# Kernel optimization log

Hardware: AMD Instinct MI355X
Metric: run time of the kernel (lower is better)

Reference implementation:

```python
import jax, jax.numpy as jnp
import numpy as np

N_U = 100000   # user nodes
N_V = 100000   # item nodes
D = 64         # input_dim
O = 64         # output_dim
R = 5          # num_support (rating levels)
E = 500000     # edges per relation


def setup_inputs() -> dict:
    key = jax.random.key(0)
    ks = jax.random.split(key, 8)
    init_range = np.sqrt(6.0 / (D + O))
    return {
        "x_u": jax.random.normal(ks[0], (N_U, D), jnp.float32),
        "x_v": jax.random.normal(ks[1], (N_V, D), jnp.float32),
        "weights_u": jax.random.uniform(ks[2], (R, D, O), jnp.float32, -init_range, init_range),
        "weights_v": jax.random.uniform(ks[3], (R, D, O), jnp.float32, -init_range, init_range),
        "bias_u": jnp.full((O,), 0.01, jnp.float32),
        "bias_v": jnp.full((O,), 0.01, jnp.float32),
        "edge_val": jax.random.uniform(ks[4], (R, E), jnp.float32),
        "edge_u": jax.random.randint(ks[5], (R, E), 0, N_U, jnp.int32),
        "edge_v": jax.random.randint(ks[6], (R, E), 0, N_V, jnp.int32),
    }


def reference(x_u, x_v, weights_u, weights_v, bias_u, bias_v, edge_val, edge_u, edge_v):
    # Cumulative (ordinal mixture) weights: wu_i = sum_{j<=i} W_u[j]
    Wu = jnp.cumsum(weights_u, axis=0)          # [R, D, O]
    Wv = jnp.cumsum(weights_v, axis=0)          # [R, D, O]

    tmp_u = jnp.einsum("nd,rdo->rno", x_u, Wu)  # [R, N_U, O]
    tmp_v = jnp.einsum("md,rdo->rmo", x_v, Wv)  # [R, N_V, O]

    gather = jax.vmap(lambda t, idx: t[idx])    # per-relation row gather

    # z_u = sum_r support_r @ tmp_v_r : scatter edge messages into user rows
    msg_u = (edge_val[..., None] * gather(tmp_v, edge_v)).reshape(R * E, O)
    z_u = jax.ops.segment_sum(msg_u, edge_u.reshape(-1), num_segments=N_U)

    # z_v = sum_r support_r^T @ tmp_u_r : scatter into item rows
    msg_v = (edge_val[..., None] * gather(tmp_u, edge_u)).reshape(R * E, O)
    z_v = jax.ops.segment_sum(msg_v, edge_v.reshape(-1), num_segments=N_V)

    u_out = jax.nn.relu(z_u + bias_u)
    v_out = jax.nn.relu(z_v + bias_v)
    return (u_out, v_out)
```

## Files before the change

kernel.cpp:

```cpp
#include <hip/hip_runtime.h>

#define N_U 100000
#define N_V 100000
#define OO 64
#define RR 5
#define EE 500000
#define TOT_E (RR * EE)
#define NB 782
#define CAP 4096
#define CAPU 3584

typedef short bf16x8 __attribute__((ext_vector_type(8)));
typedef float f32x4 __attribute__((ext_vector_type(4)));

__device__ __forceinline__ float bf2f(unsigned short u) {
  union { unsigned int i; float f; } x;
  x.i = ((unsigned int)u) << 16;
  return x.f;
}
__device__ __forceinline__ unsigned short f2bf(float f) {
  union { float f; unsigned int i; } x;
  x.f = f;
  unsigned int lsb = (x.i >> 16) & 1u;
  unsigned int r = x.i + 0x7fffu + lsb;
  return (unsigned short)(r >> 16);
}

__global__ void prep_weights(const float* __restrict__ wu,
                             const float* __restrict__ wv,
                             unsigned short* __restrict__ bfrag) {
  int side = blockIdx.x;
  const float* w = side ? wv : wu;
  for (int idx = threadIdx.x; idx < 4096; idx += 256) {
    int d = idx >> 6, o = idx & 63;
    int c = o >> 4, n = o & 15;
    int sk = d >> 5, q = (d >> 3) & 3, jj = d & 7;
    int f = c * 2 + sk;
    int lane = q * 16 + n;
    int pos = (f * 64 + lane) * 8 + jj;
    float acc = 0.f;
    for (int r = 0; r < RR; ++r) {
      acc += w[r * 4096 + idx];
      bfrag[(side * RR + r) * 4096 + pos] = f2bf(acc);
    }
  }
}

__global__ __launch_bounds__(256) void gemm5_kernel(
    const float* __restrict__ X,
    const unsigned short* __restrict__ bfrag_side,
    unsigned short* __restrict__ tmp5) {
  __shared__ unsigned short smem[RR * 4096];
  for (int idx = threadIdx.x; idx < RR * 4096; idx += 256)
    smem[idx] = bfrag_side[idx];
  __syncthreads();

  int lane = threadIdx.x & 63;
  int wave = threadIdx.x >> 6;
  int q = lane >> 4, m = lane & 15;
  int t = blockIdx.x * 4 + wave;
  if (t >= N_U / 16) return;
  int r0 = t * 16;

  const float* xr = X + (size_t)(r0 + m) * 64;
  float4 p0 = *(const float4*)(xr + q * 8);
  float4 p1 = *(const float4*)(xr + q * 8 + 4);
  float4 p2 = *(const float4*)(xr + 32 + q * 8);
  float4 p3 = *(const float4*)(xr + 32 + q * 8 + 4);
  bf16x8 a0, a1;
  a0[0] = (short)f2bf(p0.x); a0[1] = (short)f2bf(p0.y);
  a0[2] = (short)f2bf(p0.z); a0[3] = (short)f2bf(p0.w);
  a0[4] = (short)f2bf(p1.x); a0[5] = (short)f2bf(p1.y);
  a0[6] = (short)f2bf(p1.z); a0[7] = (short)f2bf(p1.w);
  a1[0] = (short)f2bf(p2.x); a1[1] = (short)f2bf(p2.y);
  a1[2] = (short)f2bf(p2.z); a1[3] = (short)f2bf(p2.w);
  a1[4] = (short)f2bf(p3.x); a1[5] = (short)f2bf(p3.y);
  a1[6] = (short)f2bf(p3.z); a1[7] = (short)f2bf(p3.w);

  for (int r = 0; r < RR; ++r) {
    f32x4 acc[4];
#pragma unroll
    for (int c = 0; c < 4; ++c) {
      bf16x8 b0 = *(const bf16x8*)(smem + r * 4096 + ((c * 2 + 0) * 64 + lane) * 8);
      bf16x8 b1 = *(const bf16x8*)(smem + r * 4096 + ((c * 2 + 1) * 64 + lane) * 8);
      f32x4 a = {0.f, 0.f, 0.f, 0.f};
      a = __builtin_amdgcn_mfma_f32_16x16x32_bf16(a0, b0, a, 0, 0, 0);
      a = __builtin_amdgcn_mfma_f32_16x16x32_bf16(a1, b1, a, 0, 0, 0);
      acc[c] = a;
    }
    unsigned short* trow = tmp5 + (size_t)r * N_U * 64;
#pragma unroll
    for (int i = 0; i < 4; ++i) {
      ushort4 o;
      o.x = f2bf(acc[0][i]); o.y = f2bf(acc[1][i]);
      o.z = f2bf(acc[2][i]); o.w = f2bf(acc[3][i]);
      *(ushort4*)(trow + (size_t)(r0 + q * 4 + i) * 64 + m * 4) = o;
    }
  }
}

__global__ void init_cursor(unsigned* __restrict__ g) {
  int i = blockIdx.x * 256 + threadIdx.x;
  if (i < NB) g[i] = (unsigned)i * CAP;
}

__global__ __launch_bounds__(1024) void bucket_scatter(
    const int* __restrict__ dst, const int* __restrict__ src,
    const float* __restrict__ val, unsigned* __restrict__ gcursor,
    unsigned* __restrict__ keyP, unsigned short* __restrict__ valP) {
  __shared__ unsigned skey[8192];
  __shared__ unsigned short sval[8192];
  __shared__ unsigned short sbid[8192];
  __shared__ unsigned cnt[NB];
  __shared__ unsigned sc[1024];
  __shared__ unsigned gbase[NB];
  int tid = threadIdx.x;
  for (int i = tid; i < NB; i += 1024) cnt[i] = 0u;
  __syncthreads();
  int base = blockIdx.x * 8192;
  int t8 = base + tid * 8;
  bool full = (t8 < TOT_E);
  if (full) {
    int4 d0 = *(const int4*)(dst + t8);
    int4 d1 = *(const int4*)(dst + t8 + 4);
    atomicAdd(&cnt[d0.x >> 7], 1u);
    atomicAdd(&cnt[d0.y >> 7], 1u);
    atomicAdd(&cnt[d0.z >> 7], 1u);
    atomicAdd(&cnt[d0.w >> 7], 1u);
    atomicAdd(&cnt[d1.x >> 7], 1u);
    atomicAdd(&cnt[d1.y >> 7], 1u);
    atomicAdd(&cnt[d1.z >> 7], 1u);
    atomicAdd(&cnt[d1.w >> 7], 1u);
  }
  __syncthreads();
  sc[tid] = (tid < NB) ? cnt[tid] : 0u;
  __syncthreads();
  for (int off = 1; off < 1024; off <<= 1) {
    unsigned a = sc[tid];
    unsigned b = (tid >= off) ? sc[tid - off] : 0u;
    __syncthreads();
    sc[tid] = a + b;
    __syncthreads();
  }
  for (int b = tid; b < NB; b += 1024) {
    unsigned c = cnt[b];
    gbase[b] = c ? atomicAdd(&gcursor[b], c) : 0u;
    cnt[b] = sc[b] - c;
  }
  __syncthreads();
  unsigned total = sc[NB - 1];
  __syncthreads();
  for (int b = tid; b < NB; b += 1024) sc[b] = cnt[b];
  __syncthreads();
  if (full) {
    int4 d0 = *(const int4*)(dst + t8);
    int4 d1 = *(const int4*)(dst + t8 + 4);
    int4 s0 = *(const int4*)(src + t8);
    int4 s1 = *(const int4*)(src + t8 + 4);
    float4 v0 = *(const float4*)(val + t8);
    float4 v1 = *(const float4*)(val + t8 + 4);
    unsigned rb = (unsigned)(t8 / EE) * N_U;
#define PUT(dd, ss, vv)                                                     \
    {                                                                       \
      int bb = (dd) >> 7;                                                   \
      unsigned pos = atomicAdd(&sc[bb], 1u);                                \
      skey[pos] = (((unsigned)((dd) & 127)) << 19) | (rb + (unsigned)(ss)); \
      sval[pos] = f2bf(vv);                                                 \
      sbid[pos] = (unsigned short)bb;                                       \
    }
    PUT(d0.x, s0.x, v0.x)
    PUT(d0.y, s0.y, v0.y)
    PUT(d0.z, s0.z, v0.z)
    PUT(d0.w, s0.w, v0.w)
    PUT(d1.x, s1.x, v1.x)
    PUT(d1.y, s1.y, v1.y)
    PUT(d1.z, s1.z, v1.z)
    PUT(d1.w, s1.w, v1.w)
#undef PUT
  }
  __syncthreads();
  for (int i = tid; i < (int)total; i += 1024) {
    unsigned b = sbid[i];
    unsigned addr = gbase[b] + ((unsigned)i - cnt[b]);
    keyP[addr] = skey[i];
    valP[addr] = sval[i];
  }
}

__global__ __launch_bounds__(512, 8) void bucket_sort_agg(
    const unsigned* __restrict__ keyP, const unsigned short* __restrict__ valP,
    const unsigned* __restrict__ gcursor,
    const unsigned short* __restrict__ tmp5,
    const float* __restrict__ bias, float* __restrict__ out) {
  __shared__ unsigned okey[CAP];
  __shared__ unsigned short oval[CAP];
  __shared__ unsigned hist[128];
  __shared__ unsigned starts[129];
  __shared__ unsigned cur[128];
  int b = blockIdx.x;
  unsigned base = (unsigned)b * CAP;
  int cnt = (int)(gcursor[b] - base);
  if (cnt > CAPU) cnt = CAPU;
  for (int i = threadIdx.x; i < 128; i += 512) hist[i] = 0u;
  __syncthreads();
  for (int i = threadIdx.x; i < cnt; i += 512)
    atomicAdd(&hist[keyP[base + i] >> 19], 1u);
  __syncthreads();
  if (threadIdx.x == 0) {
    unsigned acc = 0u;
    for (int l = 0; l < 128; ++l) {
      starts[l] = acc;
      acc += (hist[l] + 3u) & ~3u;
    }
    starts[128] = acc;
  }
  __syncthreads();
  unsigned tot = starts[128];
  for (int i = threadIdx.x; i < (int)tot; i += 512) { okey[i] = 0u; oval[i] = 0; }
  for (int l = threadIdx.x; l < 128; l += 512) cur[l] = starts[l];
  __syncthreads();
  for (int i = threadIdx.x; i < cnt; i += 512) {
    unsigned k = keyP[base + i];
    unsigned pos = atomicAdd(&cur[k >> 19], 1u);
    okey[pos] = k & 0x7FFFFu;
    oval[pos] = valP[base + i];
  }
  __syncthreads();

  int lane = threadIdx.x & 63;
  int wave = threadIdx.x >> 6;
  int g16 = lane >> 4;
  int m = lane & 15;
  int nb0 = b * 128;
  int nodes = (N_U - nb0 < 128) ? (N_U - nb0) : 128;
  const unsigned short* tp = tmp5 + (m << 2);
  float bl = bias[lane];
  for (int l = wave; l < nodes; l += 8) {
    unsigned s = starts[l];
    unsigned e = starts[l + 1];
    float a0 = 0.f, a1 = 0.f, a2 = 0.f, a3 = 0.f;
    unsigned k = s;
    for (; k + 8 <= e; k += 8) {
      unsigned key0 = okey[k + g16];
      unsigned key1 = okey[k + 4 + g16];
      float v0 = bf2f(oval[k + g16]);
      float v1 = bf2f(oval[k + 4 + g16]);
      ushort4 t0 = *(const ushort4*)(tp + (size_t)key0 * 64);
      ushort4 t1 = *(const ushort4*)(tp + (size_t)key1 * 64);
      a0 += v0 * bf2f(t0.x);
      a1 += v0 * bf2f(t0.y);
      a2 += v0 * bf2f(t0.z);
      a3 += v0 * bf2f(t0.w);
      a0 += v1 * bf2f(t1.x);
      a1 += v1 * bf2f(t1.y);
      a2 += v1 * bf2f(t1.z);
      a3 += v1 * bf2f(t1.w);
    }
    if (k < e) {
      unsigned key0 = okey[k + g16];
      float v0 = bf2f(oval[k + g16]);
      ushort4 t0 = *(const ushort4*)(tp + (size_t)key0 * 64);
      a0 += v0 * bf2f(t0.x);
      a1 += v0 * bf2f(t0.y);
      a2 += v0 * bf2f(t0.z);
      a3 += v0 * bf2f(t0.w);
    }
    a0 += __shfl_xor(a0, 16); a0 += __shfl_xor(a0, 32);
    a1 += __shfl_xor(a1, 16); a1 += __shfl_xor(a1, 32);
    a2 += __shfl_xor(a2, 16); a2 += __shfl_xor(a2, 32);
    a3 += __shfl_xor(a3, 16); a3 += __shfl_xor(a3, 32);
    float r = (g16 & 2) ? ((g16 & 1) ? a3 : a2) : ((g16 & 1) ? a1 : a0);
    out[(size_t)(nb0 + l) * 64 + lane] = fmaxf(r + bl, 0.f);
  }
}

__global__ __launch_bounds__(256) void gemm_kernel(
    const float* __restrict__ X, const unsigned short* __restrict__ bfrag,
    unsigned short* __restrict__ tmp) {
  int lane = threadIdx.x & 63;
  int wave = threadIdx.x >> 6;
  int q = lane >> 4, m = lane & 15;
  bf16x8 bf[8];
#pragma unroll
  for (int f = 0; f < 8; ++f)
    bf[f] = *(const bf16x8*)(bfrag + (f * 64 + lane) * 8);
  int t = blockIdx.x * 4 + wave;
  if (t >= N_U / 16) return;
  int r0 = t * 16;
  const float* xr = X + (size_t)(r0 + m) * 64;
  float4 p0 = *(const float4*)(xr + q * 8);
  float4 p1 = *(const float4*)(xr + q * 8 + 4);
  float4 p2 = *(const float4*)(xr + 32 + q * 8);
  float4 p3 = *(const float4*)(xr + 32 + q * 8 + 4);
  bf16x8 a0, a1;
  a0[0] = (short)f2bf(p0.x); a0[1] = (short)f2bf(p0.y);
  a0[2] = (short)f2bf(p0.z); a0[3] = (short)f2bf(p0.w);
  a0[4] = (short)f2bf(p1.x); a0[5] = (short)f2bf(p1.y);
  a0[6] = (short)f2bf(p1.z); a0[7] = (short)f2bf(p1.w);
  a1[0] = (short)f2bf(p2.x); a1[1] = (short)f2bf(p2.y);
  a1[2] = (short)f2bf(p2.z); a1[3] = (short)f2bf(p2.w);
  a1[4] = (short)f2bf(p3.x); a1[5] = (short)f2bf(p3.y);
  a1[6] = (short)f2bf(p3.z); a1[7] = (short)f2bf(p3.w);
#pragma unroll
  for (int c = 0; c < 4; ++c) {
    f32x4 acc = {0.f, 0.f, 0.f, 0.f};
    acc = __builtin_amdgcn_mfma_f32_16x16x32_bf16(a0, bf[c * 2 + 0], acc, 0, 0, 0);
    acc = __builtin_amdgcn_mfma_f32_16x16x32_bf16(a1, bf[c * 2 + 1], acc, 0, 0, 0);
#pragma unroll
    for (int i = 0; i < 4; ++i)
      tmp[(size_t)(r0 + q * 4 + i) * 64 + c * 16 + m] = f2bf(acc[i]);
  }
}

__global__ __launch_bounds__(256) void scatter_kernel(
    const unsigned short* __restrict__ tmp, const float* __restrict__ edge_val,
    const int* __restrict__ dst_idx, const int* __restrict__ src_idx,
    float* __restrict__ z, int base, int cnt) {
  int e = blockIdx.x * 4 + (threadIdx.x >> 6);
  int j = threadIdx.x & 63;
  int d = dst_idx[e] - base;
  if ((unsigned)d >= (unsigned)cnt) return;
  int s = src_idx[e];
  float w = edge_val[e];
  atomicAdd(&z[(size_t)d * 64 + j], w * bf2f(tmp[(size_t)s * 64 + j]));
}

__global__ __launch_bounds__(256) void finalize_kernel(
    const float* __restrict__ z, const float* __restrict__ bias,
    float* __restrict__ out) {
  size_t i4 = ((size_t)blockIdx.x * 256 + threadIdx.x) * 4;
  float4 zz = *(const float4*)(z + i4);
  const float4 bb = *(const float4*)(bias + (i4 & 63));
  float4 o;
  o.x = fmaxf(zz.x + bb.x, 0.f);
  o.y = fmaxf(zz.y + bb.y, 0.f);
  o.z = fmaxf(zz.z + bb.z, 0.f);
  o.w = fmaxf(zz.w + bb.w, 0.f);
  *(float4*)(out + i4) = o;
}

extern "C" void kernel_launch(void* const* d_in, const int* in_sizes, int n_in,
                              void* d_out, int out_size, void* d_ws, size_t ws_size,
                              hipStream_t stream) {
  const float* x_u      = (const float*)d_in[0];
  const float* x_v      = (const float*)d_in[1];
  const float* w_u      = (const float*)d_in[2];
  const float* w_v      = (const float*)d_in[3];
  const float* bias_u   = (const float*)d_in[4];
  const float* bias_v   = (const float*)d_in[5];
  const float* edge_val = (const float*)d_in[6];
  const int*   edge_u   = (const int*)d_in[7];
  const int*   edge_v   = (const int*)d_in[8];
  float* out = (float*)d_out;
  char* ws = (char*)d_ws;

  const size_t FAST_NEED = 83763200;

  unsigned short* bfrag = (unsigned short*)ws;
  prep_weights<<<2, 256, 0, stream>>>(w_u, w_v, bfrag);

  if (ws_size >= FAST_NEED) {
    unsigned short* tmp5      = (unsigned short*)(ws + 131072);
    unsigned*       gcursor   = (unsigned*)(ws + 64131072);
    unsigned*       keyP      = (unsigned*)(ws + 64544768);
    unsigned short* valP      = (unsigned short*)(ws + 77357056);

    const int edge_grid = (TOT_E + 8191) / 8192;
    const int gemm_grid = (N_U / 16 + 3) / 4;

    for (int side = 0; side < 2; ++side) {
      const float* X = side ? x_u : x_v;
      const unsigned short* frag0 = bfrag + (side ? 0 : RR * 4096);
      const int* dst = side ? edge_v : edge_u;
      const int* src = side ? edge_u : edge_v;
      const float* bias = side ? bias_v : bias_u;
      float* out_side = out + (size_t)side * N_U * OO;

      init_cursor<<<4, 256, 0, stream>>>(gcursor);
      bucket_scatter<<<edge_grid, 1024, 0, stream>>>(dst, src, edge_val, gcursor,
                                                     keyP, valP);
      gemm5_kernel<<<gemm_grid, 256, 0, stream>>>(X, frag0, tmp5);
      bucket_sort_agg<<<NB, 512, 0, stream>>>(keyP, valP, gcursor, tmp5, bias,
                                              out_side);
    }
    return;
  }

  unsigned short* tmp = (unsigned short*)(ws + 131072);
  float*          z   = (float*)(ws + 131072 + 12800000);
  const size_t fixed = 131072 + 12800000;
  size_t zbytes = ws_size > fixed ? ws_size - fixed : 0;
  long chunk = (long)(zbytes / (OO * 4));
  chunk -= chunk % 16;
  if (chunk < 16) chunk = 16;
  if (chunk > N_U) chunk = N_U;

  const int gemm_grid = (N_U / 16 + 3) / 4;
  const int scat_grid = EE / 4;

  for (int side = 0; side < 2; ++side) {
    const float* X = side ? x_u : x_v;
    const unsigned short* frag0 = bfrag + (side ? 0 : RR * 4096);
    const int* dst = side ? edge_v : edge_u;
    const int* src = side ? edge_u : edge_v;
    const float* bias = side ? bias_v : bias_u;
    float* out_side = out + (size_t)side * N_U * OO;

    for (long base = 0; base < N_U; base += chunk) {
      long cnt = N_U - base < chunk ? N_U - base : chunk;
      hipMemsetAsync(z, 0, (size_t)cnt * OO * 4, stream);
      for (int r = 0; r < RR; ++r) {
        gemm_kernel<<<gemm_grid, 256, 0, stream>>>(X, frag0 + r * 4096, tmp);
        scatter_kernel<<<scat_grid, 256, 0, stream>>>(
            tmp, edge_val + (size_t)r * EE, dst + (size_t)r * EE,
            src + (size_t)r * EE, z, (int)base, (int)cnt);
      }
      finalize_kernel<<<(int)(cnt / 16), 256, 0, stream>>>(
          z, bias, out_side + base * OO);
    }
  }
}
```

Baseline: 337.9 us.

## Fuse bucket scatter and GEMM into one heterogeneous launch, fold cursor init

Merges the edge bucket-scatter kernel and the per-relation GEMM into a single launch: the first 306 blocks do the scatter and the rest run the MFMA GEMM with 1024-thread blocks of 16 waves. Cursor initialisation for both sides moves into prep_weights, using a separate cursor array per side, so the per-side init launches go away. This removes launch gaps and lets the memory-bound scatter overlap with the GEMM. The cost is that GEMM blocks now hold the larger shared-memory allocation and 1024 threads, which may reduce occupancy.

```diff
diff --git a/kernel.cpp b/kernel.cpp
--- a/kernel.cpp
+++ b/kernel.cpp
@@ -9,6 +9,8 @@
 #define NB 782
 #define CAP 4096
 #define CAPU 3584
+#define SCAT_BLOCKS 306
+#define GEMM_BLOCKS 391
 
 typedef short bf16x8 __attribute__((ext_vector_type(8)));
 typedef float f32x4 __attribute__((ext_vector_type(4)));
@@ -28,8 +30,13 @@
 
 __global__ void prep_weights(const float* __restrict__ wu,
                              const float* __restrict__ wv,
-                             unsigned short* __restrict__ bfrag) {
+                             unsigned short* __restrict__ bfrag,
+                             unsigned* __restrict__ gcur) {
   int side = blockIdx.x;
+  if (gcur) {
+    unsigned* g = gcur + side * 1024;
+    for (int i = threadIdx.x; i < NB; i += 256) g[i] = (unsigned)i * CAP;
+  }
   const float* w = side ? wv : wu;
   for (int idx = threadIdx.x; idx < 4096; idx += 256) {
     int d = idx >> 6, o = idx & 63;
@@ -46,144 +53,138 @@
   }
 }
 
-__global__ __launch_bounds__(256) void gemm5_kernel(
+__global__ __launch_bounds__(1024) void scatter_gemm(
+    const int* __restrict__ dst, const int* __restrict__ src,
+    const float* __restrict__ val, unsigned* __restrict__ gcursor,
+    unsigned* __restrict__ keyP, unsigned short* __restrict__ valP,
     const float* __restrict__ X,
     const unsigned short* __restrict__ bfrag_side,
     unsigned short* __restrict__ tmp5) {
-  __shared__ unsigned short smem[RR * 4096];
-  for (int idx = threadIdx.x; idx < RR * 4096; idx += 256)
-    smem[idx] = bfrag_side[idx];
-  __syncthreads();
-
-  int lane = threadIdx.x & 63;
-  int wave = threadIdx.x >> 6;
-  int q = lane >> 4, m = lane & 15;
-  int t = blockIdx.x * 4 + wave;
-  if (t >= N_U / 16) return;
-  int r0 = t * 16;
-
-  const float* xr = X + (size_t)(r0 + m) * 64;
-  float4 p0 = *(const float4*)(xr + q * 8);
-  float4 p1 = *(const float4*)(xr + q * 8 + 4);
-  float4 p2 = *(const float4*)(xr + 32 + q * 8);
-  float4 p3 = *(const float4*)(xr + 32 + q * 8 + 4);
-  bf16x8 a0, a1;
-  a0[0] = (short)f2bf(p0.x); a0[1] = (short)f2bf(p0.y);
-  a0[2] = (short)f2bf(p0.z); a0[3] = (short)f2bf(p0.w);
-  a0[4] = (short)f2bf(p1.x); a0[5] = (short)f2bf(p1.y);
-  a0[6] = (short)f2bf(p1.z); a0[7] = (short)f2bf(p1.w);
-  a1[0] = (short)f2bf(p2.x); a1[1] = (short)f2bf(p2.y);
-  a1[2] = (short)f2bf(p2.z); a1[3] = (short)f2bf(p2.w);
-  a1[4] = (short)f2bf(p3.x); a1[5] = (short)f2bf(p3.y);
-  a1[6] = (short)f2bf(p3.z); a1[7] = (short)f2bf(p3.w);
-
-  for (int r = 0; r < RR; ++r) {
-    f32x4 acc[4];
+  __shared__ unsigned lds_u32[18972];
+  int blk = blockIdx.x;
+  int tid = threadIdx.x;
+  if (blk < SCAT_BLOCKS) {
+    unsigned* skey = lds_u32;
+    unsigned short* sval = (unsigned short*)(lds_u32 + 8192);
+    unsigned short* sbid = (unsigned short*)(lds_u32 + 12288);
+    unsigned* cnt  = lds_u32 + 16384;
+    unsigned* sc   = lds_u32 + 17166;
+    unsigned* gbase = lds_u32 + 18190;
+    for (int i = tid; i < NB; i += 1024) cnt[i] = 0u;
+    __syncthreads();
+    int base = blk * 8192;
+    int t8 = base + tid * 8;
+    bool full = (t8 < TOT_E);
+    if (full) {
+      int4 d0 = *(const int4*)(dst + t8);
+      int4 d1 = *(const int4*)(dst + t8 + 4);
+      atomicAdd(&cnt[d0.x >> 7], 1u);
+      atomicAdd(&cnt[d0.y >> 7], 1u);
+      atomicAdd(&cnt[d0.z >> 7], 1u);
+      atomicAdd(&cnt[d0.w >> 7], 1u);
+      atomicAdd(&cnt[d1.x >> 7], 1u);
+      atomicAdd(&cnt[d1.y >> 7], 1u);
+      atomicAdd(&cnt[d1.z >> 7], 1u);
+      atomicAdd(&cnt[d1.w >> 7], 1u);
+    }
+    __syncthreads();
+    sc[tid] = (tid < NB) ? cnt[tid] : 0u;
+    __syncthreads();
+    for (int off = 1; off < 1024; off <<= 1) {
+      unsigned a = sc[tid];
+      unsigned b = (tid >= off) ? sc[tid - off] : 0u;
+      __syncthreads();
+      sc[tid] = a + b;
+      __syncthreads();
+    }
+    for (int b = tid; b < NB; b += 1024) {
+      unsigned c = cnt[b];
+      gbase[b] = c ? atomicAdd(&gcursor[b], c) : 0u;
+      cnt[b] = sc[b] - c;
+    }
+    __syncthreads();
+    unsigned total = sc[NB - 1];
+    __syncthreads();
+    for (int b = tid; b < NB; b += 1024) sc[b] = cnt[b];
+    __syncthreads();
+    if (full) {
+      int4 d0 = *(const int4*)(dst + t8);
+      int4 d1 = *(const int4*)(dst + t8 + 4);
+      int4 s0 = *(const int4*)(src + t8);
+      int4 s1 = *(const int4*)(src + t8 + 4);
+      float4 v0 = *(const float4*)(val + t8);
+      float4 v1 = *(const float4*)(val + t8 + 4);
+      unsigned rb = (unsigned)(t8 / EE) * N_U;
+#define PUT(dd, ss, vv)                                                     \
+      {                                                                     \
+        int bb = (dd) >> 7;                                                 \
+        unsigned pos = atomicAdd(&sc[bb], 1u);                              \
+        skey[pos] = (((unsigned)((dd) & 127)) << 19) | (rb + (unsigned)(ss)); \
+        sval[pos] = f2bf(vv);                                               \
+        sbid[pos] = (unsigned short)bb;                                     \
+      }
+      PUT(d0.x, s0.x, v0.x)
+      PUT(d0.y, s0.y, v0.y)
+      PUT(d0.z, s0.z, v0.z)
+      PUT(d0.w, s0.w, v0.w)
+      PUT(d1.x, s1.x, v1.x)
+      PUT(d1.y, s1.y, v1.y)
+      PUT(d1.z, s1.z, v1.z)
+      PUT(d1.w, s1.w, v1.w)
+#undef PUT
+    }
+    __syncthreads();
+    for (int i = tid; i < (int)total; i += 1024) {
+      unsigned b = sbid[i];
+      unsigned addr = gbase[b] + ((unsigned)i - cnt[b]);
+      keyP[addr] = skey[i];
+      valP[addr] = sval[i];
+    }
+  } else {
+    unsigned short* smem = (unsigned short*)lds_u32;
+    for (int i = tid; i < 2560; i += 1024)
+      ((bf16x8*)smem)[i] = ((const bf16x8*)bfrag_side)[i];
+    __syncthreads();
+    int lane = tid & 63;
+    int wave = tid >> 6;
+    int q = lane >> 4, m = lane & 15;
+    int t = (blk - SCAT_BLOCKS) * 16 + wave;
+    if (t >= N_U / 16) return;
+    int r0 = t * 16;
+    const float* xr = X + (size_t)(r0 + m) * 64;
+    float4 p0 = *(const float4*)(xr + q * 8);
+    float4 p1 = *(const float4*)(xr + q * 8 + 4);
+    float4 p2 = *(const float4*)(xr + 32 + q * 8);
+    float4 p3 = *(const float4*)(xr + 32 + q * 8 + 4);
+    bf16x8 a0, a1;
+    a0[0] = (short)f2bf(p0.x); a0[1] = (short)f2bf(p0.y);
+    a0[2] = (short)f2bf(p0.z); a0[3] = (short)f2bf(p0.w);
+    a0[4] = (short)f2bf(p1.x); a0[5] = (short)f2bf(p1.y);
+    a0[6] = (short)f2bf(p1.z); a0[7] = (short)f2bf(p1.w);
+    a1[0] = (short)f2bf(p2.x); a1[1] = (short)f2bf(p2.y);
+    a1[2] = (short)f2bf(p2.z); a1[3] = (short)f2bf(p2.w);
+    a1[4] = (short)f2bf(p3.x); a1[5] = (short)f2bf(p3.y);
+    a1[6] = (short)f2bf(p3.z); a1[7] = (short)f2bf(p3.w);
+    for (int r = 0; r < RR; ++r) {
+      f32x4 acc[4];
 #pragma unroll
-    for (int c = 0; c < 4; ++c) {
-      bf16x8 b0 = *(const bf16x8*)(smem + r * 4096 + ((c * 2 + 0) * 64 + lane) * 8);
-      bf16x8 b1 = *(const bf16x8*)(smem + r * 4096 + ((c * 2 + 1) * 64 + lane) * 8);
-      f32x4 a = {0.f, 0.f, 0.f, 0.f};
-      a = __builtin_amdgcn_mfma_f32_16x16x32_bf16(a0, b0, a, 0, 0, 0);
-      a = __builtin_amdgcn_mfma_f32_16x16x32_bf16(a1, b1, a, 0, 0, 0);
-      acc[c] = a;
-    }
-    unsigned short* trow = tmp5 + (size_t)r * N_U * 64;
+      for (int c = 0; c < 4; ++c) {
+        bf16x8 b0 = *(const bf16x8*)(smem + r * 4096 + ((c * 2 + 0) * 64 + lane) * 8);
+        bf16x8 b1 = *(const bf16x8*)(smem + r * 4096 + ((c * 2 + 1) * 64 + lane) * 8);
+        f32x4 a = {0.f, 0.f, 0.f, 0.f};
+        a = __builtin_amdgcn_mfma_f32_16x16x32_bf16(a0, b0, a, 0, 0, 0);
+        a = __builtin_amdgcn_mfma_f32_16x16x32_bf16(a1, b1, a, 0, 0, 0);
+        acc[c] = a;
+      }
+      unsigned short* trow = tmp5 + (size_t)r * N_U * 64;
 #pragma unroll
-    for (int i = 0; i < 4; ++i) {
-      ushort4 o;
-      o.x = f2bf(acc[0][i]); o.y = f2bf(acc[1][i]);
-      o.z = f2bf(acc[2][i]); o.w = f2bf(acc[3][i]);
-      *(ushort4*)(trow + (size_t)(r0 + q * 4 + i) * 64 + m * 4) = o;
-    }
-  }
-}
-
-__global__ void init_cursor(unsigned* __restrict__ g) {
-  int i = blockIdx.x * 256 + threadIdx.x;
-  if (i < NB) g[i] = (unsigned)i * CAP;
-}
-
-__global__ __launch_bounds__(1024) void bucket_scatter(
-    const int* __restrict__ dst, const int* __restrict__ src,
-    const float* __restrict__ val, unsigned* __restrict__ gcursor,
-    unsigned* __restrict__ keyP, unsigned short* __restrict__ valP) {
-  __shared__ unsigned skey[8192];
-  __shared__ unsigned short sval[8192];
-  __shared__ unsigned short sbid[8192];
-  __shared__ unsigned cnt[NB];
-  __shared__ unsigned sc[1024];
-  __shared__ unsigned gbase[NB];
-  int tid = threadIdx.x;
-  for (int i = tid; i < NB; i += 1024) cnt[i] = 0u;
-  __syncthreads();
-  int base = blockIdx.x * 8192;
-  int t8 = base + tid * 8;
-  bool full = (t8 < TOT_E);
-  if (full) {
-    int4 d0 = *(const int4*)(dst + t8);
-    int4 d1 = *(const int4*)(dst + t8 + 4);
-    atomicAdd(&cnt[d0.x >> 7], 1u);
-    atomicAdd(&cnt[d0.y >> 7], 1u);
-    atomicAdd(&cnt[d0.z >> 7], 1u);
-    atomicAdd(&cnt[d0.w >> 7], 1u);
-    atomicAdd(&cnt[d1.x >> 7], 1u);
-    atomicAdd(&cnt[d1.y >> 7], 1u);
-    atomicAdd(&cnt[d1.z >> 7], 1u);
-    atomicAdd(&cnt[d1.w >> 7], 1u);
-  }
-  __syncthreads();
-  sc[tid] = (tid < NB) ? cnt[tid] : 0u;
-  __syncthreads();
-  for (int off = 1; off < 1024; off <<= 1) {
-    unsigned a = sc[tid];
-    unsigned b = (tid >= off) ? sc[tid - off] : 0u;
-    __syncthreads();
-    sc[tid] = a + b;
-    __syncthreads();
-  }
-  for (int b = tid; b < NB; b += 1024) {
-    unsigned c = cnt[b];
-    gbase[b] = c ? atomicAdd(&gcursor[b], c) : 0u;
-    cnt[b] = sc[b] - c;
-  }
-  __syncthreads();
-  unsigned total = sc[NB - 1];
-  __syncthreads();
-  for (int b = tid; b < NB; b += 1024) sc[b] = cnt[b];
-  __syncthreads();
-  if (full) {
-    int4 d0 = *(const int4*)(dst + t8);
-    int4 d1 = *(const int4*)(dst + t8 + 4);
-    int4 s0 = *(const int4*)(src + t8);
-    int4 s1 = *(const int4*)(src + t8 + 4);
-    float4 v0 = *(const float4*)(val + t8);
-    float4 v1 = *(const float4*)(val + t8 + 4);
-    unsigned rb = (unsigned)(t8 / EE) * N_U;
-#define PUT(dd, ss, vv)                                                     \
-    {                                                                       \
-      int bb = (dd) >> 7;                                                   \
-      unsigned pos = atomicAdd(&sc[bb], 1u);                                \
-      skey[pos] = (((unsigned)((dd) & 127)) << 19) | (rb + (unsigned)(ss)); \
-      sval[pos] = f2bf(vv);                                                 \
-      sbid[pos] = (unsigned short)bb;                                       \
-    }
-    PUT(d0.x, s0.x, v0.x)
-    PUT(d0.y, s0.y, v0.y)
-    PUT(d0.z, s0.z, v0.z)
-    PUT(d0.w, s0.w, v0.w)
-    PUT(d1.x, s1.x, v1.x)
-    PUT(d1.y, s1.y, v1.y)
-    PUT(d1.z, s1.z, v1.z)
-    PUT(d1.w, s1.w, v1.w)
-#undef PUT
-  }
-  __syncthreads();
-  for (int i = tid; i < (int)total; i += 1024) {
-    unsigned b = sbid[i];
-    unsigned addr = gbase[b] + ((unsigned)i - cnt[b]);
-    keyP[addr] = skey[i];
-    valP[addr] = sval[i];
+      for (int i = 0; i < 4; ++i) {
+        ushort4 o;
+        o.x = f2bf(acc[0][i]); o.y = f2bf(acc[1][i]);
+        o.z = f2bf(acc[2][i]); o.w = f2bf(acc[3][i]);
+        *(ushort4*)(trow + (size_t)(r0 + q * 4 + i) * 64 + m * 4) = o;
+      }
+    }
   }
 }
 
@@ -357,16 +358,14 @@
   const size_t FAST_NEED = 83763200;
 
   unsigned short* bfrag = (unsigned short*)ws;
-  prep_weights<<<2, 256, 0, stream>>>(w_u, w_v, bfrag);
 
   if (ws_size >= FAST_NEED) {
-    unsigned short* tmp5      = (unsigned short*)(ws + 131072);
-    unsigned*       gcursor   = (unsigned*)(ws + 64131072);
-    unsigned*       keyP      = (unsigned*)(ws + 64544768);
-    unsigned short* valP      = (unsigned short*)(ws + 77357056);
-
-    const int edge_grid = (TOT_E + 8191) / 8192;
-    const int gemm_grid = (N_U / 16 + 3) / 4;
+    unsigned short* tmp5 = (unsigned short*)(ws + 131072);
+    unsigned*       gcur = (unsigned*)(ws + 64131072);
+    unsigned*       keyP = (unsigned*)(ws + 64544768);
+    unsigned short* valP = (unsigned short*)(ws + 77357056);
+
+    prep_weights<<<2, 256, 0, stream>>>(w_u, w_v, bfrag, gcur);
 
     for (int side = 0; side < 2; ++side) {
       const float* X = side ? x_u : x_v;
@@ -375,16 +374,17 @@
       const int* src = side ? edge_u : edge_v;
       const float* bias = side ? bias_v : bias_u;
       float* out_side = out + (size_t)side * N_U * OO;
-
-      init_cursor<<<4, 256, 0, stream>>>(gcursor);
-      bucket_scatter<<<edge_grid, 1024, 0, stream>>>(dst, src, edge_val, gcursor,
-                                                     keyP, valP);
-      gemm5_kernel<<<gemm_grid, 256, 0, stream>>>(X, frag0, tmp5);
-      bucket_sort_agg<<<NB, 512, 0, stream>>>(keyP, valP, gcursor, tmp5, bias,
+      unsigned* gc = gcur + side * 1024;
+
+      scatter_gemm<<<SCAT_BLOCKS + GEMM_BLOCKS, 1024, 0, stream>>>(
+          dst, src, edge_val, gc, keyP, valP, X, frag0, tmp5);
+      bucket_sort_agg<<<NB, 512, 0, stream>>>(keyP, valP, gc, tmp5, bias,
                                               out_side);
     }
     return;
   }
+
+  prep_weights<<<2, 256, 0, stream>>>(w_u, w_v, bfrag, (unsigned*)0);
 
   unsigned short* tmp = (unsigned short*)(ws + 131072);
   float*          z   = (float*)(ws + 131072 + 12800000);
```

Result: faster. 322.2 us (-4.7%).
